# Performance work log

Measured on AMD Instinct MI355X. Metric: run time of the kernel, lower is better.

## Reference

```python
import jax, jax.numpy as jnp
import numpy as np

NUM_HEADS = 32
NUM_KV_HEADS = 8
HEAD_DIM = 128
SCALE = 0.08838834764831845  # 1/sqrt(128)
NUM_SEQS = 8
BLKS_PER_SEQ = 64
MEM_BLOCK_SIZE = 32          # ctx_len = 64*32 = 2048 per sequence
Q_LEN = 64                   # active diffusion block per sequence
N_BLOCKS = 1024


def setup_inputs() -> dict:
    key = jax.random.key(0)
    k1, k2, k3, k4, k5 = jax.random.split(key, 5)
    T = NUM_SEQS * Q_LEN
    q = jax.random.normal(k1, (T, NUM_HEADS * HEAD_DIM), dtype=jnp.float32)
    k = jax.random.normal(k2, (T, NUM_KV_HEADS * HEAD_DIM), dtype=jnp.float32)
    v = jax.random.normal(k3, (T, NUM_KV_HEADS * HEAD_DIM), dtype=jnp.float32)
    k_cache = jax.random.normal(k4, (N_BLOCKS, MEM_BLOCK_SIZE, NUM_KV_HEADS, HEAD_DIM), dtype=jnp.float32)
    v_cache = jax.random.normal(k5, (N_BLOCKS, MEM_BLOCK_SIZE, NUM_KV_HEADS, HEAD_DIM), dtype=jnp.float32)
    # each sequence owns a distinct contiguous set of cache blocks
    block_tables = jnp.arange(NUM_SEQS * BLKS_PER_SEQ, dtype=jnp.int32).reshape(NUM_SEQS, BLKS_PER_SEQ)
    return {"q": q, "k": k, "v": v, "k_cache": k_cache, "v_cache": v_cache,
            "block_tables": block_tables}


def reference(q, k, v, k_cache, v_cache, block_tables):
    S, B = block_tables.shape
    ctx_len = B * MEM_BLOCK_SIZE
    G = NUM_HEADS // NUM_KV_HEADS  # GQA group size

    # reshape flattened token streams: [T, H*D] -> [S, L, H, D]
    qh = q.reshape(S, Q_LEN, NUM_KV_HEADS, G, HEAD_DIM)
    kn = k.reshape(S, Q_LEN, NUM_KV_HEADS, HEAD_DIM)
    vn = v.reshape(S, Q_LEN, NUM_KV_HEADS, HEAD_DIM)

    # paged gather: block_tables -> [S, B, MEM_BLK, Hkv, D] -> [S, ctx_len, Hkv, D]
    kc = k_cache[block_tables].reshape(S, ctx_len, NUM_KV_HEADS, HEAD_DIM)
    vc = v_cache[block_tables].reshape(S, ctx_len, NUM_KV_HEADS, HEAD_DIM)

    # packed KV = gathered context ++ new active-block tokens (load_kvcache kernel)
    K = jnp.concatenate([kc, kn], axis=1)  # [S, ctx_len+Q_LEN, Hkv, D]
    V = jnp.concatenate([vc, vn], axis=1)

    # diffusion-LM mask: active block attends bidirectionally to full context + itself
    scores = jnp.einsum('sqhgd,skhd->shgqk', qh, K) * SCALE
    probs = jax.nn.softmax(scores, axis=-1)
    out = jnp.einsum('shgqk,skhd->sqhgd', probs, V)
    return out.reshape(S * Q_LEN, NUM_HEADS * HEAD_DIM)
```

## Files before the change

kernel.cpp:

```cpp
#include <hip/hip_runtime.h>

#define GQA 4
#define Q_LEN 64
#define SCALE 0.08838834764831845f
#define RLN2 1.4426950408889634f
#define NTILES 66
#define CACHE_TILES 64

typedef __attribute__((ext_vector_type(4))) float f4;
typedef __attribute__((ext_vector_type(4))) float f32x4;
typedef __attribute__((ext_vector_type(8))) short short8;
typedef __attribute__((ext_vector_type(4))) unsigned int u32x4;

__device__ __forceinline__ unsigned cvt_pk(float lo, float hi) {
  unsigned r;
  asm("v_cvt_pk_bf16_f32 %0, %1, %2" : "=v"(r) : "v"(lo), "v"(hi));
  return r;
}
__device__ __forceinline__ unsigned short f2bf(float f) {
  unsigned u = __builtin_bit_cast(unsigned, f);
  u += 0x7fffu + ((u >> 16) & 1u);
  return (unsigned short)(u >> 16);
}

#define K_OFF  0
#define V_OFF  8192
#define P_OFF  18432
#define BT_OFF 23552
#define LDS_BYTES 23808

__device__ __forceinline__ unsigned k_addr(int key, int d) {
  return (unsigned)(key * 256 + ((d * 2) ^ ((key & 7) << 4)));
}
__device__ __forceinline__ unsigned v_addr(int d, int key) {
  return (unsigned)(d * 80 + key * 2);
}

__global__ __launch_bounds__(256, 4)
void attn_partial(const float* __restrict__ q, const float* __restrict__ kn,
                  const float* __restrict__ vn, const float* __restrict__ kc,
                  const float* __restrict__ vc, const int* __restrict__ btab,
                  float* __restrict__ part_o, float* __restrict__ part_ml,
                  float* __restrict__ out, int nc)
{
  __shared__ __align__(16) char lds[LDS_BYTES];
  const int bid  = blockIdx.x;
  const int c    = bid >> 8;
  const int rest = bid & 255;
  const int g = rest >> 6, s = (rest >> 3) & 7, h = rest & 7;
  const int tid  = threadIdx.x;
  const int wave = tid >> 6, lane = tid & 63;
  const int lhi  = lane >> 4, llo = lane & 15;

  const int base  = NTILES / nc, rem = NTILES % nc;
  const int start = c * base + (c < rem ? c : rem);
  const int nt    = base + (c < rem ? 1 : 0);

  if (tid < 64) *(int*)(lds + BT_OFF + tid * 4) = btab[s * CACHE_TILES + tid];

  short8 qf[4];
  {
    const float qsc = SCALE * RLN2;
    const float* qrow = q + (size_t)(s * Q_LEN + wave * 16 + llo) * 4096 + (h * GQA + g) * 128;
#pragma unroll
    for (int cc = 0; cc < 4; ++cc) {
      const float* p = qrow + cc * 32 + lhi * 8;
      f4 a = *(const f4*)p; f4 b = *(const f4*)(p + 4);
      u32x4 w;
      w[0] = cvt_pk(a[0] * qsc, a[1] * qsc); w[1] = cvt_pk(a[2] * qsc, a[3] * qsc);
      w[2] = cvt_pk(b[0] * qsc, b[1] * qsc); w[3] = cvt_pk(b[2] * qsc, b[3] * qsc);
      qf[cc] = __builtin_bit_cast(short8, w);
    }
  }

  f32x4 of[8];
#pragma unroll
  for (int i = 0; i < 8; ++i) of[i] = (f32x4){0.f, 0.f, 0.f, 0.f};
  float m_run[4], l_run[4];
#pragma unroll
  for (int r = 0; r < 4; ++r) { m_run[r] = -1e30f; l_run[r] = 0.f; }

  const int ktk = tid >> 3;
  const int kc0 = (tid & 7) * 16;
  const int vdq = (tid >> 3) * 4;
  const int vkp = tid & 7;
  const size_t k_toff = (size_t)ktk * 1024 + h * 128 + kc0;
  const size_t v_off0 = (size_t)(2 * vkp) * 1024 + h * 128 + vdq;

  f4 rk[4], rv[4];
  auto issue_loads = [&](int tile) {
    const float *kb_, *vb_;
    if (tile < CACHE_TILES) {
      const int pb = *(const int*)(lds + BT_OFF + tile * 4);
      kb_ = kc + (size_t)pb * 32768;
      vb_ = vc + (size_t)pb * 32768;
    } else {
      const size_t row0 = (size_t)(s * Q_LEN + (tile - CACHE_TILES) * 32) * 1024;
      kb_ = kn + row0;
      vb_ = vn + row0;
    }
    rk[0] = *(const f4*)(kb_ + k_toff);
    rk[1] = *(const f4*)(kb_ + k_toff + 4);
    rk[2] = *(const f4*)(kb_ + k_toff + 8);
    rk[3] = *(const f4*)(kb_ + k_toff + 12);
    rv[0] = *(const f4*)(vb_ + v_off0);
    rv[1] = *(const f4*)(vb_ + v_off0 + 1024);
    rv[2] = *(const f4*)(vb_ + v_off0 + 16384);
    rv[3] = *(const f4*)(vb_ + v_off0 + 17408);
  };
  auto write_tile = [&]() {
    u32x4 w0, w1;
    w0[0] = cvt_pk(rk[0][0], rk[0][1]); w0[1] = cvt_pk(rk[0][2], rk[0][3]);
    w0[2] = cvt_pk(rk[1][0], rk[1][1]); w0[3] = cvt_pk(rk[1][2], rk[1][3]);
    w1[0] = cvt_pk(rk[2][0], rk[2][1]); w1[1] = cvt_pk(rk[2][2], rk[2][3]);
    w1[2] = cvt_pk(rk[3][0], rk[3][1]); w1[3] = cvt_pk(rk[3][2], rk[3][3]);
    *(u32x4*)(lds + K_OFF + k_addr(ktk, kc0))     = w0;
    *(u32x4*)(lds + K_OFF + k_addr(ktk, kc0 + 8)) = w1;
#pragma unroll
    for (int i = 0; i < 4; ++i) {
      *(unsigned*)(lds + V_OFF + v_addr(vdq + i, 2 * vkp))      = cvt_pk(rv[0][i], rv[1][i]);
      *(unsigned*)(lds + V_OFF + v_addr(vdq + i, 2 * vkp + 16)) = cvt_pk(rv[2][i], rv[3][i]);
    }
  };

  __syncthreads();
  issue_loads(start);
  write_tile();
  __syncthreads();

  for (int it = 0; it < nt; ++it) {
    if (it + 1 < nt) issue_loads(start + it + 1);

    {
      f32x4 s0 = {0.f,0.f,0.f,0.f}, s1 = {0.f,0.f,0.f,0.f};
#pragma unroll
      for (int cc = 0; cc < 4; ++cc) {
        short8 kf0 = *(const short8*)(lds + K_OFF + k_addr(llo,      cc * 32 + lhi * 8));
        short8 kf1 = *(const short8*)(lds + K_OFF + k_addr(llo + 16, cc * 32 + lhi * 8));
        s0 = __builtin_amdgcn_mfma_f32_16x16x32_bf16(qf[cc], kf0, s0, 0, 0, 0);
        s1 = __builtin_amdgcn_mfma_f32_16x16x32_bf16(qf[cc], kf1, s1, 0, 0, 0);
      }
      float p0[4], p1[4], tred[4];
#pragma unroll
      for (int r = 0; r < 4; ++r) tred[r] = fmaxf(s0[r], s1[r]);
#pragma unroll
      for (int off = 1; off < 16; off <<= 1)
#pragma unroll
        for (int r = 0; r < 4; ++r) tred[r] = fmaxf(tred[r], __shfl_xor(tred[r], off, 64));

      bool grow = (tred[0] > m_run[0]) | (tred[1] > m_run[1]) |
                  (tred[2] > m_run[2]) | (tred[3] > m_run[3]);
      const int resc = __any((int)grow);
      float corr[4];
      if (resc) {
#pragma unroll
        for (int r = 0; r < 4; ++r) {
          const float mnew = fmaxf(m_run[r], tred[r]);
          corr[r] = exp2f(m_run[r] - mnew);
          m_run[r] = mnew;
        }
      }
#pragma unroll
      for (int r = 0; r < 4; ++r) {
        p0[r] = exp2f(s0[r] - m_run[r]);
        p1[r] = exp2f(s1[r] - m_run[r]);
        tred[r] = p0[r] + p1[r];
      }
#pragma unroll
      for (int off = 1; off < 16; off <<= 1)
#pragma unroll
        for (int r = 0; r < 4; ++r) tred[r] += __shfl_xor(tred[r], off, 64);
      if (resc) {
#pragma unroll
        for (int r = 0; r < 4; ++r) l_run[r] = l_run[r] * corr[r] + tred[r];
#pragma unroll
        for (int dc = 0; dc < 8; ++dc)
#pragma unroll
          for (int r = 0; r < 4; ++r) of[dc][r] *= corr[r];
      } else {
#pragma unroll
        for (int r = 0; r < 4; ++r) l_run[r] += tred[r];
      }

      char* pb_ = lds + P_OFF + wave * 1280;
#pragma unroll
      for (int r = 0; r < 4; ++r) {
        const int row = lhi * 4 + r;
        *(unsigned short*)(pb_ + row * 80 + llo * 2)        = f2bf(p0[r]);
        *(unsigned short*)(pb_ + row * 80 + (llo + 16) * 2) = f2bf(p1[r]);
      }
      short8 pa = *(const short8*)(pb_ + llo * 80 + lhi * 16);
#pragma unroll
      for (int dc = 0; dc < 8; ++dc) {
        short8 vf = *(const short8*)(lds + V_OFF + v_addr(dc * 16 + llo, lhi * 8));
        of[dc] = __builtin_amdgcn_mfma_f32_16x16x32_bf16(pa, vf, of[dc], 0, 0, 0);
      }
    }

    __syncthreads();
    if (it + 1 < nt) {
      write_tile();
      __syncthreads();
    }
  }

  if (nc == 1) {
    float inv[4];
#pragma unroll
    for (int r = 0; r < 4; ++r) inv[r] = 1.f / l_run[r];
#pragma unroll
    for (int dc = 0; dc < 8; ++dc)
#pragma unroll
      for (int r = 0; r < 4; ++r)
        out[(size_t)(s * Q_LEN + wave * 16 + lhi * 4 + r) * 4096
            + (size_t)((h * GQA + g) * 128 + dc * 16 + llo)] = of[dc][r] * inv[r];
  } else {
#pragma unroll
    for (int dc = 0; dc < 8; ++dc)
#pragma unroll
      for (int r = 0; r < 4; ++r) {
        const int row = wave * 16 + lhi * 4 + r;
        part_o[((size_t)bid * 64 + row) * 128 + dc * 16 + llo] = of[dc][r];
      }
    if (llo == 0) {
#pragma unroll
      for (int r = 0; r < 4; ++r) {
        const int row = wave * 16 + lhi * 4 + r;
        part_ml[(size_t)bid * 128 + row]      = m_run[r];
        part_ml[(size_t)bid * 128 + 64 + row] = l_run[r];
      }
    }
  }
}

template<int NC>
__global__ __launch_bounds__(256)
void merge_k(const float* __restrict__ po, const float* __restrict__ pml,
             float* __restrict__ out)
{
  const int t   = blockIdx.x * 256 + threadIdx.x;
  const int d4  = t & 31;
  const int hh  = (t >> 5) & 31;
  const int tok = t >> 10;
  const int s = tok >> 6, row = tok & 63, h = hh >> 2, g = hh & 3;

  float m[NC], l[NC]; f4 o[NC];
  float M = -1e30f;
#pragma unroll
  for (int c = 0; c < NC; ++c) {
    const int bid = c * 256 + g * 64 + s * 8 + h;
    m[c] = pml[(size_t)bid * 128 + row];
    l[c] = pml[(size_t)bid * 128 + 64 + row];
    o[c] = *(const f4*)&po[((size_t)bid * 64 + row) * 128 + d4 * 4];
    M = fmaxf(M, m[c]);
  }
  f4 num = {0.f,0.f,0.f,0.f};
  float den = 0.f;
#pragma unroll
  for (int c = 0; c < NC; ++c) {
    const float w = exp2f(m[c] - M);
    num += w * o[c];
    den += w * l[c];
  }
  const float inv = 1.f / den;
  *(f4*)&out[(size_t)tok * 4096 + hh * 128 + d4 * 4] = num * inv;
}

extern "C" void kernel_launch(void* const* d_in, const int* in_sizes, int n_in,
                              void* d_out, int out_size, void* d_ws, size_t ws_size,
                              hipStream_t stream) {
  (void)in_sizes; (void)n_in; (void)out_size;
  const float* q  = (const float*)d_in[0];
  const float* k  = (const float*)d_in[1];
  const float* v  = (const float*)d_in[2];
  const float* kc = (const float*)d_in[3];
  const float* vc = (const float*)d_in[4];
  const int* bt   = (const int*)d_in[5];
  float* out = (float*)d_out;

  const size_t per_chunk = 256ull * 64 * 128 * 4 + 256ull * 128 * 4;
  int NC = 1;
  if (ws_size >= 4 * per_chunk) NC = 4;
  else if (ws_size >= 2 * per_chunk) NC = 2;

  float* po  = (float*)d_ws;
  float* pml = po + (size_t)NC * 256 * 64 * 128;

  attn_partial<<<dim3(NC * 256), dim3(256), 0, stream>>>(q, k, v, kc, vc, bt, po, pml, out, NC);
  if (NC == 4)      merge_k<4><<<dim3(2048), dim3(256), 0, stream>>>(po, pml, out);
  else if (NC == 2) merge_k<2><<<dim3(2048), dim3(256), 0, stream>>>(po, pml, out);
}
```

Measured before the change: 302.6 us.

## Double-buffer K/V LDS tiles with two-deep register prefetch and MFMA priority

Splits the K/V shared-memory staging into two buffers and keeps two tiles of global loads in flight in registers. The loop alternates buffers so the next tile's LDS write overlaps the current compute, which cuts one of the two barriers per tile. MFMA sections are raised to a higher wave priority, and the barrier is a custom lgkmcnt wait with sched barriers. LDS use and register pressure grow, so launch bounds drop from 4 to 3 blocks per CU and occupancy falls. Loads past the last tile are clamped to the last tile, which adds redundant memory traffic.

```diff
diff --git a/kernel.cpp b/kernel.cpp
--- a/kernel.cpp
+++ b/kernel.cpp
@@ -23,11 +23,12 @@
   return (unsigned short)(u >> 16);
 }
 
-#define K_OFF  0
-#define V_OFF  8192
-#define P_OFF  18432
-#define BT_OFF 23552
-#define LDS_BYTES 23808
+#define KBUF   8192
+#define V0_OFF 16384
+#define VBUF   10240
+#define P_OFF  36864
+#define BT_OFF 41984
+#define LDS_BYTES 42240
 
 __device__ __forceinline__ unsigned k_addr(int key, int d) {
   return (unsigned)(key * 256 + ((d * 2) ^ ((key & 7) << 4)));
@@ -36,7 +37,11 @@
   return (unsigned)(d * 80 + key * 2);
 }
 
-__global__ __launch_bounds__(256, 4)
+#define SCHED0() __builtin_amdgcn_sched_barrier(0)
+#define BAR() do { asm volatile("s_waitcnt lgkmcnt(0)" ::: "memory"); SCHED0(); \
+                   __builtin_amdgcn_s_barrier(); SCHED0(); } while (0)
+
+__global__ __launch_bounds__(256, 3)
 void attn_partial(const float* __restrict__ q, const float* __restrict__ kn,
                   const float* __restrict__ vn, const float* __restrict__ kc,
                   const float* __restrict__ vc, const int* __restrict__ btab,
@@ -55,6 +60,7 @@
   const int base  = NTILES / nc, rem = NTILES % nc;
   const int start = c * base + (c < rem ? c : rem);
   const int nt    = base + (c < rem ? 1 : 0);
+  const int tlast = start + nt - 1;
 
   if (tid < 64) *(int*)(lds + BT_OFF + tid * 4) = btab[s * CACHE_TILES + tid];
 
@@ -87,8 +93,9 @@
   const size_t k_toff = (size_t)ktk * 1024 + h * 128 + kc0;
   const size_t v_off0 = (size_t)(2 * vkp) * 1024 + h * 128 + vdq;
 
-  f4 rk[4], rv[4];
-  auto issue_loads = [&](int tile) {
+  f4 rkA[4], rvA[4], rkB[4], rvB[4];
+
+  auto issue_loads = [&](int tile, f4* rk, f4* rv) {
     const float *kb_, *vb_;
     if (tile < CACHE_TILES) {
       const int pb = *(const int*)(lds + BT_OFF + tile * 4);
@@ -108,100 +115,113 @@
     rv[2] = *(const f4*)(vb_ + v_off0 + 16384);
     rv[3] = *(const f4*)(vb_ + v_off0 + 17408);
   };
-  auto write_tile = [&]() {
+  auto write_tile = [&](int sel, const f4* rk, const f4* rv) {
     u32x4 w0, w1;
     w0[0] = cvt_pk(rk[0][0], rk[0][1]); w0[1] = cvt_pk(rk[0][2], rk[0][3]);
     w0[2] = cvt_pk(rk[1][0], rk[1][1]); w0[3] = cvt_pk(rk[1][2], rk[1][3]);
     w1[0] = cvt_pk(rk[2][0], rk[2][1]); w1[1] = cvt_pk(rk[2][2], rk[2][3]);
     w1[2] = cvt_pk(rk[3][0], rk[3][1]); w1[3] = cvt_pk(rk[3][2], rk[3][3]);
-    *(u32x4*)(lds + K_OFF + k_addr(ktk, kc0))     = w0;
-    *(u32x4*)(lds + K_OFF + k_addr(ktk, kc0 + 8)) = w1;
+    char* kb = lds + sel * KBUF;
+    *(u32x4*)(kb + k_addr(ktk, kc0))     = w0;
+    *(u32x4*)(kb + k_addr(ktk, kc0 + 8)) = w1;
+    char* vb = lds + V0_OFF + sel * VBUF;
 #pragma unroll
     for (int i = 0; i < 4; ++i) {
-      *(unsigned*)(lds + V_OFF + v_addr(vdq + i, 2 * vkp))      = cvt_pk(rv[0][i], rv[1][i]);
-      *(unsigned*)(lds + V_OFF + v_addr(vdq + i, 2 * vkp + 16)) = cvt_pk(rv[2][i], rv[3][i]);
+      *(unsigned*)(vb + v_addr(vdq + i, 2 * vkp))      = cvt_pk(rv[0][i], rv[1][i]);
+      *(unsigned*)(vb + v_addr(vdq + i, 2 * vkp + 16)) = cvt_pk(rv[2][i], rv[3][i]);
     }
   };
-
-  __syncthreads();
-  issue_loads(start);
-  write_tile();
-  __syncthreads();
-
-  for (int it = 0; it < nt; ++it) {
-    if (it + 1 < nt) issue_loads(start + it + 1);
-
-    {
-      f32x4 s0 = {0.f,0.f,0.f,0.f}, s1 = {0.f,0.f,0.f,0.f};
-#pragma unroll
-      for (int cc = 0; cc < 4; ++cc) {
-        short8 kf0 = *(const short8*)(lds + K_OFF + k_addr(llo,      cc * 32 + lhi * 8));
-        short8 kf1 = *(const short8*)(lds + K_OFF + k_addr(llo + 16, cc * 32 + lhi * 8));
-        s0 = __builtin_amdgcn_mfma_f32_16x16x32_bf16(qf[cc], kf0, s0, 0, 0, 0);
-        s1 = __builtin_amdgcn_mfma_f32_16x16x32_bf16(qf[cc], kf1, s1, 0, 0, 0);
+  auto compute = [&](int sel) {
+    const char* kb = lds + sel * KBUF;
+    const char* vb = lds + V0_OFF + sel * VBUF;
+    f32x4 s0 = {0.f,0.f,0.f,0.f}, s1 = {0.f,0.f,0.f,0.f};
+    __builtin_amdgcn_s_setprio(1);
+#pragma unroll
+    for (int cc = 0; cc < 4; ++cc) {
+      short8 kf0 = *(const short8*)(kb + k_addr(llo,      cc * 32 + lhi * 8));
+      short8 kf1 = *(const short8*)(kb + k_addr(llo + 16, cc * 32 + lhi * 8));
+      s0 = __builtin_amdgcn_mfma_f32_16x16x32_bf16(qf[cc], kf0, s0, 0, 0, 0);
+      s1 = __builtin_amdgcn_mfma_f32_16x16x32_bf16(qf[cc], kf1, s1, 0, 0, 0);
+    }
+    __builtin_amdgcn_s_setprio(0);
+    float p0[4], p1[4], tred[4];
+#pragma unroll
+    for (int r = 0; r < 4; ++r) tred[r] = fmaxf(s0[r], s1[r]);
+#pragma unroll
+    for (int off = 1; off < 16; off <<= 1)
+#pragma unroll
+      for (int r = 0; r < 4; ++r) tred[r] = fmaxf(tred[r], __shfl_xor(tred[r], off, 64));
+
+    bool grow = (tred[0] > m_run[0]) | (tred[1] > m_run[1]) |
+                (tred[2] > m_run[2]) | (tred[3] > m_run[3]);
+    const int resc = __any((int)grow);
+    float corr[4];
+    if (resc) {
+#pragma unroll
+      for (int r = 0; r < 4; ++r) {
+        const float mnew = fmaxf(m_run[r], tred[r]);
+        corr[r] = exp2f(m_run[r] - mnew);
+        m_run[r] = mnew;
       }
-      float p0[4], p1[4], tred[4];
-#pragma unroll
-      for (int r = 0; r < 4; ++r) tred[r] = fmaxf(s0[r], s1[r]);
-#pragma unroll
-      for (int off = 1; off < 16; off <<= 1)
-#pragma unroll
-        for (int r = 0; r < 4; ++r) tred[r] = fmaxf(tred[r], __shfl_xor(tred[r], off, 64));
-
-      bool grow = (tred[0] > m_run[0]) | (tred[1] > m_run[1]) |
-                  (tred[2] > m_run[2]) | (tred[3] > m_run[3]);
-      const int resc = __any((int)grow);
-      float corr[4];
-      if (resc) {
-#pragma unroll
-        for (int r = 0; r < 4; ++r) {
-          const float mnew = fmaxf(m_run[r], tred[r]);
-          corr[r] = exp2f(m_run[r] - mnew);
-          m_run[r] = mnew;
-        }
-      }
-#pragma unroll
-      for (int r = 0; r < 4; ++r) {
-        p0[r] = exp2f(s0[r] - m_run[r]);
-        p1[r] = exp2f(s1[r] - m_run[r]);
-        tred[r] = p0[r] + p1[r];
-      }
-#pragma unroll
-      for (int off = 1; off < 16; off <<= 1)
-#pragma unroll
-        for (int r = 0; r < 4; ++r) tred[r] += __shfl_xor(tred[r], off, 64);
-      if (resc) {
-#pragma unroll
-        for (int r = 0; r < 4; ++r) l_run[r] = l_run[r] * corr[r] + tred[r];
-#pragma unroll
-        for (int dc = 0; dc < 8; ++dc)
-#pragma unroll
-          for (int r = 0; r < 4; ++r) of[dc][r] *= corr[r];
-      } else {
-#pragma unroll
-        for (int r = 0; r < 4; ++r) l_run[r] += tred[r];
-      }
-
-      char* pb_ = lds + P_OFF + wave * 1280;
-#pragma unroll
-      for (int r = 0; r < 4; ++r) {
-        const int row = lhi * 4 + r;
-        *(unsigned short*)(pb_ + row * 80 + llo * 2)        = f2bf(p0[r]);
-        *(unsigned short*)(pb_ + row * 80 + (llo + 16) * 2) = f2bf(p1[r]);
-      }
-      short8 pa = *(const short8*)(pb_ + llo * 80 + lhi * 16);
-#pragma unroll
-      for (int dc = 0; dc < 8; ++dc) {
-        short8 vf = *(const short8*)(lds + V_OFF + v_addr(dc * 16 + llo, lhi * 8));
-        of[dc] = __builtin_amdgcn_mfma_f32_16x16x32_bf16(pa, vf, of[dc], 0, 0, 0);
-      }
-    }
-
-    __syncthreads();
-    if (it + 1 < nt) {
-      write_tile();
-      __syncthreads();
-    }
+    }
+#pragma unroll
+    for (int r = 0; r < 4; ++r) {
+      p0[r] = exp2f(s0[r] - m_run[r]);
+      p1[r] = exp2f(s1[r] - m_run[r]);
+      tred[r] = p0[r] + p1[r];
+    }
+#pragma unroll
+    for (int off = 1; off < 16; off <<= 1)
+#pragma unroll
+      for (int r = 0; r < 4; ++r) tred[r] += __shfl_xor(tred[r], off, 64);
+    if (resc) {
+#pragma unroll
+      for (int r = 0; r < 4; ++r) l_run[r] = l_run[r] * corr[r] + tred[r];
+#pragma unroll
+      for (int dc = 0; dc < 8; ++dc)
+#pragma unroll
+        for (int r = 0; r < 4; ++r) of[dc][r] *= corr[r];
+    } else {
+#pragma unroll
+      for (int r = 0; r < 4; ++r) l_run[r] += tred[r];
+    }
+
+    char* pb_ = lds + P_OFF + wave * 1280;
+#pragma unroll
+    for (int r = 0; r < 4; ++r) {
+      const int row = lhi * 4 + r;
+      *(unsigned short*)(pb_ + row * 80 + llo * 2)        = f2bf(p0[r]);
+      *(unsigned short*)(pb_ + row * 80 + (llo + 16) * 2) = f2bf(p1[r]);
+    }
+    short8 pa = *(const short8*)(pb_ + llo * 80 + lhi * 16);
+    __builtin_amdgcn_s_setprio(1);
+#pragma unroll
+    for (int dc = 0; dc < 8; ++dc) {
+      short8 vf = *(const short8*)(vb + v_addr(dc * 16 + llo, lhi * 8));
+      of[dc] = __builtin_amdgcn_mfma_f32_16x16x32_bf16(pa, vf, of[dc], 0, 0, 0);
+    }
+    __builtin_amdgcn_s_setprio(0);
+  };
+
+  auto tclamp = [&](int t) { return t > tlast ? tlast : t; };
+
+  BAR();
+  issue_loads(tclamp(start),     rkA, rvA);
+  issue_loads(tclamp(start + 1), rkB, rvB);
+  write_tile(0, rkA, rvA);
+  issue_loads(tclamp(start + 2), rkA, rvA);
+  BAR();
+
+  for (int it = 0; it < nt; it += 2) {
+    compute(0);
+    write_tile(1, rkB, rvB);
+    issue_loads(tclamp(start + it + 3), rkB, rvB);
+    BAR();
+    if (it + 1 >= nt) break;
+    compute(1);
+    write_tile(0, rkA, rvA);
+    issue_loads(tclamp(start + it + 4), rkA, rvA);
+    BAR();
   }
 
   if (nc == 1) {
```

After: 456.1 us. 50.7% more time.

## Transpose QK MFMA so P stays in registers, dropping the LDS P round-trip

Applied to the files above, without the earlier changes.

The kernel swaps the MFMA operand order so the score tile comes out transposed, with each lane holding a single query row. This lets the row max and row sum use two cross-lane shuffles instead of four-step butterfly reductions over four rows. The bf16 probabilities are packed straight into the A operand of the PV MFMA, which removes the per-tile LDS write and read of P along with its scratch buffer. To keep the keys in the right order, the V tile is stored in LDS with a permuted key-slot layout. Running max and sum become per-lane scalars, and shuffles redistribute them for rescaling and the final normalisation.

```diff
diff --git a/kernel.cpp b/kernel.cpp
--- a/kernel.cpp
+++ b/kernel.cpp
@@ -17,23 +17,17 @@
   asm("v_cvt_pk_bf16_f32 %0, %1, %2" : "=v"(r) : "v"(lo), "v"(hi));
   return r;
 }
-__device__ __forceinline__ unsigned short f2bf(float f) {
-  unsigned u = __builtin_bit_cast(unsigned, f);
-  u += 0x7fffu + ((u >> 16) & 1u);
-  return (unsigned short)(u >> 16);
-}
 
 #define K_OFF  0
 #define V_OFF  8192
-#define P_OFF  18432
-#define BT_OFF 23552
-#define LDS_BYTES 23808
+#define BT_OFF 18432
+#define LDS_BYTES 18688
 
 __device__ __forceinline__ unsigned k_addr(int key, int d) {
   return (unsigned)(key * 256 + ((d * 2) ^ ((key & 7) << 4)));
 }
-__device__ __forceinline__ unsigned v_addr(int d, int key) {
-  return (unsigned)(d * 80 + key * 2);
+__device__ __forceinline__ unsigned v_addr(int d, int slot) {
+  return (unsigned)(d * 80 + slot * 2);
 }
 
 __global__ __launch_bounds__(256, 4)
@@ -76,14 +70,13 @@
   f32x4 of[8];
 #pragma unroll
   for (int i = 0; i < 8; ++i) of[i] = (f32x4){0.f, 0.f, 0.f, 0.f};
-  float m_run[4], l_run[4];
-#pragma unroll
-  for (int r = 0; r < 4; ++r) { m_run[r] = -1e30f; l_run[r] = 0.f; }
+  float m_run = -1e30f, l_run = 0.f;
 
   const int ktk = tid >> 3;
   const int kc0 = (tid & 7) * 16;
   const int vdq = (tid >> 3) * 4;
   const int vkp = tid & 7;
+  const int vslot = (vkp >> 1) * 8 + (vkp & 1) * 2;
   const size_t k_toff = (size_t)ktk * 1024 + h * 128 + kc0;
   const size_t v_off0 = (size_t)(2 * vkp) * 1024 + h * 128 + vdq;
 
@@ -118,8 +111,8 @@
     *(u32x4*)(lds + K_OFF + k_addr(ktk, kc0 + 8)) = w1;
 #pragma unroll
     for (int i = 0; i < 4; ++i) {
-      *(unsigned*)(lds + V_OFF + v_addr(vdq + i, 2 * vkp))      = cvt_pk(rv[0][i], rv[1][i]);
-      *(unsigned*)(lds + V_OFF + v_addr(vdq + i, 2 * vkp + 16)) = cvt_pk(rv[2][i], rv[3][i]);
+      *(unsigned*)(lds + V_OFF + v_addr(vdq + i, vslot))     = cvt_pk(rv[0][i], rv[1][i]);
+      *(unsigned*)(lds + V_OFF + v_addr(vdq + i, vslot + 4)) = cvt_pk(rv[2][i], rv[3][i]);
     }
   };
 
@@ -137,59 +130,48 @@
       for (int cc = 0; cc < 4; ++cc) {
         short8 kf0 = *(const short8*)(lds + K_OFF + k_addr(llo,      cc * 32 + lhi * 8));
         short8 kf1 = *(const short8*)(lds + K_OFF + k_addr(llo + 16, cc * 32 + lhi * 8));
-        s0 = __builtin_amdgcn_mfma_f32_16x16x32_bf16(qf[cc], kf0, s0, 0, 0, 0);
-        s1 = __builtin_amdgcn_mfma_f32_16x16x32_bf16(qf[cc], kf1, s1, 0, 0, 0);
-      }
-      float p0[4], p1[4], tred[4];
-#pragma unroll
-      for (int r = 0; r < 4; ++r) tred[r] = fmaxf(s0[r], s1[r]);
-#pragma unroll
-      for (int off = 1; off < 16; off <<= 1)
-#pragma unroll
-        for (int r = 0; r < 4; ++r) tred[r] = fmaxf(tred[r], __shfl_xor(tred[r], off, 64));
-
-      bool grow = (tred[0] > m_run[0]) | (tred[1] > m_run[1]) |
-                  (tred[2] > m_run[2]) | (tred[3] > m_run[3]);
-      const int resc = __any((int)grow);
-      float corr[4];
+        s0 = __builtin_amdgcn_mfma_f32_16x16x32_bf16(kf0, qf[cc], s0, 0, 0, 0);
+        s1 = __builtin_amdgcn_mfma_f32_16x16x32_bf16(kf1, qf[cc], s1, 0, 0, 0);
+      }
+      float mx = fmaxf(fmaxf(fmaxf(s0[0], s0[1]), fmaxf(s0[2], s0[3])),
+                       fmaxf(fmaxf(s1[0], s1[1]), fmaxf(s1[2], s1[3])));
+      mx = fmaxf(mx, __shfl_xor(mx, 16, 64));
+      mx = fmaxf(mx, __shfl_xor(mx, 32, 64));
+
+      const int resc = __any((int)(mx > m_run));
+      float corr = 1.f;
       if (resc) {
+        const float mnew = fmaxf(m_run, mx);
+        corr = exp2f(m_run - mnew);
+        m_run = mnew;
+      }
+      float p0[4], p1[4];
+#pragma unroll
+      for (int r = 0; r < 4; ++r) {
+        p0[r] = exp2f(s0[r] - m_run);
+        p1[r] = exp2f(s1[r] - m_run);
+      }
+      float sum = (p0[0] + p0[1]) + (p0[2] + p0[3]) + (p1[0] + p1[1]) + (p1[2] + p1[3]);
+      sum += __shfl_xor(sum, 16, 64);
+      sum += __shfl_xor(sum, 32, 64);
+      if (resc) {
+        l_run = l_run * corr + sum;
 #pragma unroll
         for (int r = 0; r < 4; ++r) {
-          const float mnew = fmaxf(m_run[r], tred[r]);
-          corr[r] = exp2f(m_run[r] - mnew);
-          m_run[r] = mnew;
+          const float cr = __shfl(corr, lhi * 16 + lhi * 4 + r, 64);
+#pragma unroll
+          for (int dc = 0; dc < 8; ++dc) of[dc][r] *= cr;
         }
-      }
-#pragma unroll
-      for (int r = 0; r < 4; ++r) {
-        p0[r] = exp2f(s0[r] - m_run[r]);
-        p1[r] = exp2f(s1[r] - m_run[r]);
-        tred[r] = p0[r] + p1[r];
-      }
-#pragma unroll
-      for (int off = 1; off < 16; off <<= 1)
-#pragma unroll
-        for (int r = 0; r < 4; ++r) tred[r] += __shfl_xor(tred[r], off, 64);
-      if (resc) {
-#pragma unroll
-        for (int r = 0; r < 4; ++r) l_run[r] = l_run[r] * corr[r] + tred[r];
-#pragma unroll
-        for (int dc = 0; dc < 8; ++dc)
-#pragma unroll
-          for (int r = 0; r < 4; ++r) of[dc][r] *= corr[r];
       } else {
-#pragma unroll
-        for (int r = 0; r < 4; ++r) l_run[r] += tred[r];
-      }
-
-      char* pb_ = lds + P_OFF + wave * 1280;
-#pragma unroll
-      for (int r = 0; r < 4; ++r) {
-        const int row = lhi * 4 + r;
-        *(unsigned short*)(pb_ + row * 80 + llo * 2)        = f2bf(p0[r]);
-        *(unsigned short*)(pb_ + row * 80 + (llo + 16) * 2) = f2bf(p1[r]);
-      }
-      short8 pa = *(const short8*)(pb_ + llo * 80 + lhi * 16);
+        l_run += sum;
+      }
+
+      u32x4 pw;
+      pw[0] = cvt_pk(p0[0], p0[1]);
+      pw[1] = cvt_pk(p0[2], p0[3]);
+      pw[2] = cvt_pk(p1[0], p1[1]);
+      pw[3] = cvt_pk(p1[2], p1[3]);
+      const short8 pa = __builtin_bit_cast(short8, pw);
 #pragma unroll
       for (int dc = 0; dc < 8; ++dc) {
         short8 vf = *(const short8*)(lds + V_OFF + v_addr(dc * 16 + llo, lhi * 8));
@@ -207,7 +189,8 @@
   if (nc == 1) {
     float inv[4];
 #pragma unroll
-    for (int r = 0; r < 4; ++r) inv[r] = 1.f / l_run[r];
+    for (int r = 0; r < 4; ++r)
+      inv[r] = 1.f / __shfl(l_run, lhi * 16 + lhi * 4 + r, 64);
 #pragma unroll
     for (int dc = 0; dc < 8; ++dc)
 #pragma unroll
@@ -222,13 +205,9 @@
         const int row = wave * 16 + lhi * 4 + r;
         part_o[((size_t)bid * 64 + row) * 128 + dc * 16 + llo] = of[dc][r];
       }
-    if (llo == 0) {
-#pragma unroll
-      for (int r = 0; r < 4; ++r) {
-        const int row = wave * 16 + lhi * 4 + r;
-        part_ml[(size_t)bid * 128 + row]      = m_run[r];
-        part_ml[(size_t)bid * 128 + 64 + row] = l_run[r];
-      }
+    if (lhi == 0) {
+      part_ml[(size_t)bid * 128 + wave * 16 + llo]      = m_run;
+      part_ml[(size_t)bid * 128 + 64 + wave * 16 + llo] = l_run;
     }
   }
 }
```

Result: faster. 296.5 us (-2.0%).
